# Kernel optimization log

Hardware: AMD Instinct MI355X
Metric: run time of the kernel (lower is better)

Reference implementation:

```python
import jax, jax.numpy as jnp
import numpy as np

# Reference for Net.get_seed_aff_x4 (+ Sinkhorn), the custom-kernel hotspot of this
# module. The ResNet50 conv stack / side convs are standard cuDNN-covered ops and the
# external `resnet50` module is not part of this source; `feature` here is hie_fea
# (768ch at side3 resolution) and `norm_cam` is the bg-augmented CAM at the same
# resolution, exactly as they arrive at get_seed_aff_x4 in forward.

N, C, H, W, CF = 8, 21, 64, 64, 768
NUM_CLUSTERS = 2
KMEANS_ITERS = 10      # deterministic Lloyd iterations (external kmeans_pytorch is
                       # randomly initialized; we use first-two-valid-pixel init)
EPS_OT = 0.1
SINK_MAX_ITER = 100
SINK_THRESH = 0.01


def setup_inputs() -> dict:
    key = jax.random.key(0)
    k1, k2, k3 = jax.random.split(key, 3)
    norm_cam = jax.random.uniform(k1, (N, C, H, W), dtype=jnp.float32)
    label = (jax.random.uniform(k2, (N, C, 1, 1)) < 0.8).astype(jnp.float32)
    label = label.at[:, 0].set(1.0)  # background always present
    feature = jax.random.normal(k3, (N, CF, H, W), dtype=jnp.float32)
    return {"norm_cam": norm_cam, "label": label, "feature": feature}


def _kmeans_cosine(feat, feat_n, mask):
    # feat: [HW, CF] raw features, feat_n: [HW, CF] l2-normalized, mask: [HW] in {0,1}
    valid = mask > 0
    cnt = valid.sum()
    order = jnp.argsort(jnp.where(valid, 0, 1))  # stable: valid pixels first
    init = feat[order[:NUM_CLUSTERS]] * mask[order[:NUM_CLUSTERS], None]

    def step(centers, _):
        cn = centers / jnp.maximum(
            jnp.linalg.norm(centers, axis=-1, keepdims=True), 1e-8)
        sim = feat_n @ cn.T                                  # [HW, K]
        assign = jnp.argmax(sim, axis=-1)
        oh = jax.nn.one_hot(assign, NUM_CLUSTERS, dtype=feat.dtype) * mask[:, None]
        counts = oh.sum(0)
        new_c = (oh.T @ feat) / jnp.maximum(counts, 1.0)[:, None]
        return new_c, None

    centers, _ = jax.lax.scan(step, init, None, length=KMEANS_ITERS)
    # original `continue` when < num_clusters valid pixels -> centers stay zero
    return jnp.where(cnt >= NUM_CLUSTERS, centers, jnp.zeros_like(centers))


def _sinkhorn(K, u, v):
    # K: [C, M, Nk]; faithful to Net.Sinkhorn incl. early stop on mean |r - r0|
    def cond(state):
        i, r, c, err = state
        return (i < SINK_MAX_ITER) & (err >= SINK_THRESH)

    def body(state):
        i, r, c, _ = state
        r0 = r
        r = u / jnp.einsum('cmk,ck->cm', K, c)
        c = v / jnp.einsum('cmk,cm->ck', K, r)
        err = jnp.abs(r - r0).mean()
        return (i + 1, r, c, err)

    state0 = (jnp.int32(0), jnp.ones_like(u), jnp.ones_like(v),
              jnp.asarray(jnp.inf, u.dtype))
    _, r, c, _ = jax.lax.while_loop(cond, body, state0)
    return r[..., None] * c[..., None, :] * K


def reference(norm_cam, label, feature):
    n, c, h, w = norm_cam.shape
    cf = feature.shape[1]
    hw = h * w

    # seeds: one-hot argmax of norm_cam, gated by image-level labels
    belonging = jnp.argmax(norm_cam, axis=1)                       # [n,h,w]
    seeds = jnp.transpose(jax.nn.one_hot(belonging, c, dtype=norm_cam.dtype),
                          (0, 3, 1, 2)) * label                    # [n,c,h,w]
    # nearest-interp to feature size is identity (same HxW by construction)
    mask = seeds.reshape(n, c, hw)                                 # [n,c,hw]

    feat = feature.reshape(n, cf, hw).transpose(0, 2, 1)           # [n,hw,cf]
    feat_n = feat / jnp.maximum(
        jnp.linalg.norm(feat, axis=-1, keepdims=True), 1e-8)

    # per-(image, class) cosine k-means, fully vectorized (no python data loops)
    centers = jax.vmap(
        lambda f, fn, ms: jax.vmap(_kmeans_cosine, in_axes=(None, None, 0))(f, fn, ms)
    )(feat, feat_n, mask)                                          # [n,c,K,cf]
    cnt = (mask > 0).sum(-1)                                       # [n,c]

    # cosine similarity of ALL pixels to the 2 centers, mean over clusters
    centers_n = centers / jnp.maximum(
        jnp.linalg.norm(centers, axis=-1, keepdims=True), 1e-8)
    cos = jnp.einsum('nmd,nckd->nckm', feat_n, centers_n)          # [n,c,K,hw]
    cam = jnp.where((cnt >= NUM_CLUSTERS)[..., None],
                    cos.mean(axis=2), 0.0).reshape(n, c, h, w)

    # --- Sinkhorn OT refinement (torch.no_grad in original) ---
    feat_ot = feat / (jnp.linalg.norm(feat, axis=-1, keepdims=True) + 1e-5)
    cflat = centers.reshape(n, c * NUM_CLUSTERS, cf)
    cflat = cflat / (jnp.linalg.norm(cflat, axis=-1, keepdims=True) + 1e-5)
    sim = jnp.einsum('nmd,njd->nmj', feat_ot, cflat)               # [n,hw,c*K]
    # faithful to original's sim.view(M, N, n_cls).permute(2, 0, 1)
    sim = sim.reshape(n, hw, NUM_CLUSTERS, c).transpose(0, 3, 1, 2)  # [n,c,hw,K]
    Kmat = jax.lax.stop_gradient(jnp.exp(-(1.0 - sim) / EPS_OT))
    u = jnp.full((c, hw), 1.0 / hw, dtype=sim.dtype)
    v = jnp.full((c, NUM_CLUSTERS), 1.0 / NUM_CLUSTERS, dtype=sim.dtype)
    T = jax.vmap(lambda Kb: _sinkhorn(Kb, u, v))(Kmat)             # [n,c,hw,K]
    T = T.transpose(0, 1, 3, 2).reshape(n, c, NUM_CLUSTERS, h, w)

    # all_cam_maps.mean(dim=2) * label, then per-map max normalization
    out = cam * label
    out = out / (out.max(axis=(2, 3), keepdims=True) + 1e-5)
    return out, T


if __name__ == '__main__':
    o = reference(**setup_inputs())
    print(o[0].shape, o[1].shape)
```

## Files before the change

kernel.cpp:

```cpp
#include <hip/hip_runtime.h>
#include <hip/hip_bf16.h>
#include <stdint.h>

#define NIMG 8
#define NCLS 21
#define HW   4096
#define CF   768
#define NK   2
#define NJ   42
#define NJP  48
#define SINK_MAX 100

using uint32 = unsigned int;
using u16    = unsigned short;

__device__ __forceinline__ float b2f(u16 u){ union{uint32 i; float f;} x; x.i=((uint32)u)<<16; return x.f; }
__device__ __forceinline__ u16 f2b(float f){ union{float f; uint32 i;} x; x.f=f; return (u16)((x.i + 0x7fffu + ((x.i>>16)&1u))>>16); }

template<int BF>
__device__ __forceinline__ float ldin(const void* p, size_t idx){
    if (BF) return b2f(((const u16*)p)[idx]);
    return ((const float*)p)[idx];
}
template<int BF>
__device__ __forceinline__ void stout(void* p, size_t idx, float v){
    if (BF) ((u16*)p)[idx] = f2b(v);
    else    ((float*)p)[idx] = v;
}

__global__ void k_detect(const void* feat, int* flag){
    __shared__ int cnt;
    if (threadIdx.x == 0) cnt = 0;
    __syncthreads();
    const u16* f = (const u16*)feat;
    int bad = 0;
    for (int i = threadIdx.x; i < 4096; i += 256){
        int ex = (f[i] >> 7) & 0xFF;
        if (ex >= 160) bad++;
    }
    atomicAdd(&cnt, bad);
    __syncthreads();
    if (threadIdx.x == 0) *flag = (cnt < 64) ? 1 : 0;
}

template<int BF>
__global__ void k_seeds(const void* __restrict__ cam, const void* __restrict__ label,
                        int* __restrict__ pix_cls, const int* __restrict__ dflag){
    if (*dflag != BF) return;
    int g = blockIdx.x*256 + threadIdx.x;
    int n = g >> 12, p = g & 4095;
    float best = -1e30f; int bel = 0;
    for (int c = 0; c < NCLS; c++){
        float v = ldin<BF>(cam, (size_t)(n*NCLS + c)*HW + p);
        if (v > best){ best = v; bel = c; }
    }
    pix_cls[g] = (ldin<BF>(label, n*NCLS + bel) > 0.f) ? bel : -1;
}

template<int BF>
__global__ void k_norms(const void* __restrict__ feat, float* __restrict__ inv_n,
                        float* __restrict__ inv_ot, const int* __restrict__ dflag){
    if (*dflag != BF) return;
    int g = blockIdx.x*256 + threadIdx.x;
    int n = g >> 12, p = g & 4095;
    double s = 0.0;
    for (int k = 0; k < CF; k++){
        double v = (double)ldin<BF>(feat, (size_t)(n*CF + k)*HW + p);
        s += v*v;
    }
    double nr = sqrt(s);
    inv_n [g] = (float)(1.0/fmax(nr, 1e-8));
    inv_ot[g] = (float)(1.0/(nr + 1e-5));
}

template<int BF>
__global__ void k_transpose(const void* __restrict__ feat, float* __restrict__ featT,
                            const int* __restrict__ dflag){
    if (*dflag != BF) return;
    __shared__ float tile[64][65];
    int b = blockIdx.x;
    int n   = b / ((CF/64)*(HW/64));
    int rem = b % ((CF/64)*(HW/64));
    int kb = (rem / (HW/64)) * 64;
    int pb = (rem % (HW/64)) * 64;
    int tx = threadIdx.x & 63, ty = threadIdx.x >> 6;
    for (int i = 0; i < 16; i++){
        int k = ty*16 + i;
        tile[tx][k] = ldin<BF>(feat, ((size_t)(n*CF + kb + k))*HW + pb + tx);
    }
    __syncthreads();
    for (int i = 0; i < 16; i++){
        int p = ty*16 + i;
        featT[((size_t)(n*HW + pb + p))*CF + kb + tx] = tile[p][tx];
    }
}

__global__ void k_scan(const int* __restrict__ pix_cls, const float* __restrict__ featT,
                       int* __restrict__ cnt, int* __restrict__ plist,
                       double* __restrict__ centers){
    int b = blockIdx.x; int n = b / NCLS, c = b % NCLS;
    int lane = threadIdx.x;
    int* lst = plist + (size_t)b*HW;
    int count = 0, i0 = -1, i1 = -1;
    for (int base = 0; base < HW; base += 64){
        int cls = pix_cls[n*HW + base + lane];
        unsigned long long m = __ballot(cls == c);
        int pos = count + __popcll(m & ((1ull<<lane) - 1ull));
        if (cls == c) lst[pos] = base + lane;
        if (i0 < 0){
            if (m){ i0 = base + __ffsll((long long)m) - 1;
                    unsigned long long m2 = m & (m-1);
                    if (m2) i1 = base + __ffsll((long long)m2) - 1; }
        } else if (i1 < 0){
            if (m) i1 = base + __ffsll((long long)m) - 1;
        }
        count += __popcll(m);
    }
    if (lane == 0) cnt[b] = count;
    double* C0 = centers + (size_t)b*NK*CF;
    if (count >= 2){
        const float* r0 = featT + (size_t)(n*HW + i0)*CF;
        const float* r1 = featT + (size_t)(n*HW + i1)*CF;
        for (int e = lane; e < CF; e += 64){ C0[e] = (double)r0[e]; C0[CF+e] = (double)r1[e]; }
    } else {
        for (int e = lane; e < CF; e += 64){ C0[e] = 0.0; C0[CF+e] = 0.0; }
    }
}

__global__ __launch_bounds__(512, 1) void k_kmeans(const int* __restrict__ cnt,
                                                   const int* __restrict__ plist,
                                                   const float* __restrict__ featT,
                                                   double* __restrict__ centers){
    int b = blockIdx.x; int n = b / NCLS;
    int m = cnt[b];
    if (m < 2) return;
    __shared__ double Cs[2][CF];
    __shared__ float  As[2][CF];
    __shared__ double part[8][8][66];
    __shared__ double red[2];
    __shared__ float  ck[2];
    __shared__ double invn[2];
    __shared__ unsigned char asg[HW];
    __shared__ int chg;
    int tid = threadIdx.x, lane = tid & 63, w = tid >> 6;
    const int* lst = plist + (size_t)b*HW;
    double* Cg = centers + (size_t)b*NK*CF;
    for (int j = tid; j < CF; j += 512){ Cs[0][j] = Cg[j]; Cs[1][j] = Cg[CF+j]; }
    for (int i = tid; i < m; i += 512) asg[i] = 255;
    __syncthreads();
    for (int it = 0; it < 10; it++){
        if (tid < 2){ red[tid] = 0.0; ck[tid] = 0.f; }
        if (tid == 0) chg = 0;
        __syncthreads();
        double q0 = 0.0, q1 = 0.0;
        for (int j = tid; j < CF; j += 512){ q0 += Cs[0][j]*Cs[0][j]; q1 += Cs[1][j]*Cs[1][j]; }
        #pragma unroll
        for (int off = 32; off; off >>= 1){ q0 += __shfl_xor(q0, off); q1 += __shfl_xor(q1, off); }
        if (lane == 0){ atomicAdd(&red[0], q0); atomicAdd(&red[1], q1); }
        for (int j = tid; j < CF; j += 512){ As[0][j] = 0.f; As[1][j] = 0.f; }
        __syncthreads();
        if (tid == 0){
            invn[0] = 1.0/fmax(sqrt(red[0]), 1e-8);
            invn[1] = 1.0/fmax(sqrt(red[1]), 1e-8);
        }
        __syncthreads();
        double ic0 = invn[0], ic1 = invn[1];
        double c0r[12], c1r[12];
        #pragma unroll
        for (int s = 0; s < 3; s++){
            #pragma unroll
            for (int t = 0; t < 4; t++){
                int e = lane*4 + s*256 + t;
                c0r[s*4+t] = Cs[0][e];
                c1r[s*4+t] = Cs[1][e];
            }
        }
        float ac0[12], ac1[12];
        #pragma unroll
        for (int j = 0; j < 12; j++){ ac0[j] = 0.f; ac1[j] = 0.f; }
        int c0n = 0, c1n = 0, myChg = 0;
        float vA[4][12], vB[4][12];
        if (w < m){
            #pragma unroll
            for (int p = 0; p < 4; p++){
                int idx = w + 8*p; int iv = (idx < m) ? idx : (m-1);
                const float* row = featT + (size_t)(n*HW + lst[iv])*CF + lane*4;
                *(float4*)&vA[p][0] = *(const float4*)(row);
                *(float4*)&vA[p][4] = *(const float4*)(row + 256);
                *(float4*)&vA[p][8] = *(const float4*)(row + 512);
            }
        }
        for (int i = w; i < m; i += 32){
            int inext = i + 32;
            if (inext < m){
                #pragma unroll
                for (int p = 0; p < 4; p++){
                    int idx = inext + 8*p; int iv = (idx < m) ? idx : (m-1);
                    const float* row = featT + (size_t)(n*HW + lst[iv])*CF + lane*4;
                    *(float4*)&vB[p][0] = *(const float4*)(row);
                    *(float4*)&vB[p][4] = *(const float4*)(row + 256);
                    *(float4*)&vB[p][8] = *(const float4*)(row + 512);
                }
            }
            double d0[4], d1[4];
            #pragma unroll
            for (int p = 0; p < 4; p++){
                double s0 = 0.0, s1 = 0.0;
                #pragma unroll
                for (int j = 0; j < 12; j++){
                    s0 += (double)vA[p][j]*c0r[j];
                    s1 += (double)vA[p][j]*c1r[j];
                }
                d0[p] = s0; d1[p] = s1;
            }
            #pragma unroll
            for (int p = 0; p < 4; p++){
                part[w][2*p    ][lane] = d0[p];
                part[w][2*p + 1][lane] = d1[p];
            }
            asm volatile("s_waitcnt lgkmcnt(0)" ::: "memory");
            int s  = lane >> 3;
            int sub = lane & 7;
            const double* pr = &part[w][s][sub*8];
            double t = ((pr[0]+pr[1]) + (pr[2]+pr[3])) + ((pr[4]+pr[5]) + (pr[6]+pr[7]));
            t += __shfl_xor(t, 1);
            t += __shfl_xor(t, 2);
            t += __shfl_xor(t, 4);
            double tp = __shfl_xor(t, 8);
            int amine = 0;
            if ((lane & 8) == 0) amine = (t*ic0 >= tp*ic1) ? 0 : 1;
            unsigned long long bmask = __ballot(((lane & 8) == 0) && amine);
            #pragma unroll
            for (int p = 0; p < 4; p++){
                int idx = i + 8*p;
                if (idx < m){
                    int a = (int)((bmask >> (16*p)) & 1ull);
                    if (lane == 0){
                        if (asg[idx] != (unsigned char)a){ myChg++; asg[idx] = (unsigned char)a; }
                    }
                    if (a == 0){ c0n++;
                        #pragma unroll
                        for (int j = 0; j < 12; j++) ac0[j] += vA[p][j];
                    } else { c1n++;
                        #pragma unroll
                        for (int j = 0; j < 12; j++) ac1[j] += vA[p][j];
                    }
                }
            }
            #pragma unroll
            for (int p = 0; p < 4; p++){
                #pragma unroll
                for (int j = 0; j < 12; j++) vA[p][j] = vB[p][j];
            }
        }
        #pragma unroll
        for (int s = 0; s < 3; s++){
            #pragma unroll
            for (int t = 0; t < 4; t++){
                int e = lane*4 + s*256 + t;
                atomicAdd(&As[0][e], ac0[s*4+t]);
                atomicAdd(&As[1][e], ac1[s*4+t]);
            }
        }
        if (lane == 0){
            atomicAdd(&ck[0], (float)c0n); atomicAdd(&ck[1], (float)c1n);
            if (myChg) atomicAdd(&chg, myChg);
        }
        __syncthreads();
        if (chg == 0) break;
        double dv0 = fmax((double)ck[0], 1.0), dv1 = fmax((double)ck[1], 1.0);
        for (int j = tid; j < CF; j += 512){
            Cs[0][j] = (double)As[0][j]/dv0; Cs[1][j] = (double)As[1][j]/dv1;
        }
        __syncthreads();
    }
    for (int j = tid; j < CF; j += 512){ Cg[j] = Cs[0][j]; Cg[CF+j] = Cs[1][j]; }
}

__global__ void k_invc(const double* __restrict__ centers, float* __restrict__ invc_cam,
                       float* __restrict__ invc_ot){
    int b = blockIdx.x;
    int lane = threadIdx.x;
    const double* C = centers + (size_t)b*CF;
    double s = 0.0;
    for (int e = lane; e < CF; e += 64) s += C[e]*C[e];
    for (int off = 32; off; off >>= 1) s += __shfl_xor(s, off);
    if (lane == 0){
        double nr = sqrt(s);
        invc_cam[b] = (float)(1.0/fmax(nr, 1e-8));
        invc_ot[b]  = (float)(1.0/(nr + 1e-5));
    }
}

__global__ void k_cf32(const double* __restrict__ centers, float* __restrict__ Cf32){
    int n = blockIdx.x; int tid = threadIdx.x;
    for (int idx = tid; idx < NJP*CF; idx += 256){
        int j = idx / CF, e = idx - j*CF;
        float v = (j < NJ) ? (float)centers[((size_t)n*NJ + j)*CF + e] : 0.f;
        Cf32[(size_t)n*NJP*CF + idx] = v;
    }
}

__global__ __launch_bounds__(256) void k_gemmf(const float* __restrict__ featT,
                                               const float* __restrict__ Cf32,
                                               float* __restrict__ D){
    __shared__ float Fs[128][66];
    int b = blockIdx.x; int n = b >> 6; int pbase = (b & 63)*64;
    int tid = threadIdx.x, p = tid & 63;
    int jb = __builtin_amdgcn_readfirstlane((tid >> 6)*12);
    float acc[12];
    #pragma unroll
    for (int j = 0; j < 12; j++) acc[j] = 0.f;
    for (int kc = 0; kc < CF; kc += 128){
        __syncthreads();
        for (int idx = tid; idx < 64*64; idx += 256){
            int pp = idx >> 6, cw = idx & 63;
            float2 wv = *(const float2*)(featT + (size_t)(n*HW + pbase + pp)*CF + kc + cw*2);
            Fs[cw*2    ][pp] = wv.x;
            Fs[cw*2 + 1][pp] = wv.y;
        }
        __syncthreads();
        const float* Cb = Cf32 + (size_t)n*NJP*CF + kc;
        for (int k8 = 0; k8 < 128; k8 += 8){
            #pragma unroll
            for (int j = 0; j < 12; j++){
                const float* cr = Cb + (size_t)(jb + j)*CF + k8;
                #pragma unroll
                for (int k = 0; k < 8; k++)
                    acc[j] += Fs[k8 + k][p] * cr[k];
            }
        }
    }
    float* dp = D + ((size_t)(n*HW + pbase + p))*NJP + jb;
    #pragma unroll
    for (int j = 0; j < 12; j++) dp[j] = acc[j];
}

template<int BF>
__global__ __launch_bounds__(256) void k_out0(const float* __restrict__ D,
                                              const float* __restrict__ inv_n,
                                              const float* __restrict__ invc_cam,
                                              const int* __restrict__ cnt,
                                              void* __restrict__ out0,
                                              const int* __restrict__ dflag){
    if (*dflag != BF) return;
    int b = blockIdx.x; int n = b / NCLS, c = b % NCLS;
    __shared__ float wmax[4]; __shared__ float sden;
    int tid = threadIdx.x, lane = tid & 63, w = tid >> 6;
    size_t obase = (size_t)b*HW;
    if (cnt[b] < 2){
        for (int p = tid; p < HW; p += 256) stout<BF>(out0, obase + p, 0.f);
        return;
    }
    float ic0 = invc_cam[n*NJ + 2*c], ic1 = invc_cam[n*NJ + 2*c + 1];
    const float* Dn = D + (size_t)n*HW*NJP;
    float mx = -1e30f;
    for (int p = tid; p < HW; p += 256){
        const float* dp = Dn + (size_t)p*NJP + 2*c;
        float camv = 0.5f*(dp[0]*ic0 + dp[1]*ic1)*inv_n[n*HW + p];
        mx = fmaxf(mx, camv);
    }
    for (int off = 32; off; off >>= 1) mx = fmaxf(mx, __shfl_xor(mx, off));
    if (lane == 0) wmax[w] = mx;
    __syncthreads();
    if (tid == 0) sden = fmaxf(fmaxf(wmax[0], wmax[1]), fmaxf(wmax[2], wmax[3])) + 1e-5f;
    __syncthreads();
    float den = sden;
    for (int p = tid; p < HW; p += 256){
        const float* dp = Dn + (size_t)p*NJP + 2*c;
        float camv = 0.5f*(dp[0]*ic0 + dp[1]*ic1)*inv_n[n*HW + p];
        stout<BF>(out0, obase + p, camv/den);
    }
}

__global__ void k_kmat(const float* __restrict__ D, const float* __restrict__ inv_ot,
                       const float* __restrict__ invc_ot, float* __restrict__ Kg,
                       float* __restrict__ errg, int* __restrict__ arrv){
    if (blockIdx.x == 0){
        for (int i = threadIdx.x; i < NIMG*(SINK_MAX+1); i += 256){ errg[i] = 0.f; arrv[i] = 0; }
    }
    int g = blockIdx.x*256 + threadIdx.x;
    int n = g / (NCLS*HW);
    int rem = g - n*(NCLS*HW);
    int c = rem >> 12, p = rem & 4095;
    const float* dp = D + ((size_t)n*HW + p)*NJP;
    float io = inv_ot[n*HW + p];
    float s0 = dp[c]      * io * invc_ot[n*NJ + c];
    float s1 = dp[21 + c] * io * invc_ot[n*NJ + 21 + c];
    Kg[(size_t)g*2 + 0] = expf((s0 - 1.f)*10.f);
    Kg[(size_t)g*2 + 1] = expf((s1 - 1.f)*10.f);
}

template<int BF>
__global__ __launch_bounds__(256) void k_sink(const float* __restrict__ Kg,
                                              float* __restrict__ errg,
                                              int* __restrict__ arrv,
                                              void* __restrict__ d_out,
                                              const int* __restrict__ dflag){
    if (*dflag != BF) return;
    __shared__ float K0s[HW]; __shared__ float K1s[HW]; __shared__ float rs[HW];
    __shared__ float wred[4][3]; __shared__ float sh[3];
    int b = blockIdx.x; int n = b / NCLS;
    int tid = threadIdx.x, lane = tid & 63, w = tid >> 6;
    const float* Kb = Kg + (size_t)b*HW*2;
    for (int p = tid; p < HW; p += 256){ K0s[p] = Kb[p*2]; K1s[p] = Kb[p*2+1]; rs[p] = 1.f; }
    float cc0 = 1.f, cc1 = 1.f, err = 1e30f;
    const float u = 1.f/4096.f;
    int iter = 0;
    __syncthreads();
    while (iter < SINK_MAX && err >= 0.01f){
        float p0 = 0.f, p1 = 0.f, es = 0.f;
        for (int p = tid; p < HW; p += 256){
            float k0 = K0s[p], k1 = K1s[p];
            float rn = u / (k0*cc0 + k1*cc1);
            es += fabsf(rn - rs[p]);
            rs[p] = rn;
            p0 += k0*rn; p1 += k1*rn;
        }
        #pragma unroll
        for (int off = 32; off; off >>= 1){
            p0 += __shfl_xor(p0, off); p1 += __shfl_xor(p1, off); es += __shfl_xor(es, off);
        }
        if (lane == 0){ wred[w][0] = p0; wred[w][1] = p1; wred[w][2] = es; }
        __syncthreads();
        if (tid == 0){
            float P0 = wred[0][0]+wred[1][0]+wred[2][0]+wred[3][0];
            float P1 = wred[0][1]+wred[1][1]+wred[2][1]+wred[3][1];
            float ES = wred[0][2]+wred[1][2]+wred[2][2]+wred[3][2];
            sh[0] = 0.5f/P0; sh[1] = 0.5f/P1;
            int slot = n*(SINK_MAX+1) + iter;
            atomicAdd(&errg[slot], ES);
            __threadfence();
            atomicAdd(&arrv[slot], 1);
            while (__hip_atomic_load(&arrv[slot], __ATOMIC_ACQUIRE, __HIP_MEMORY_SCOPE_AGENT) < NCLS)
                __builtin_amdgcn_s_sleep(8);
            sh[2] = __hip_atomic_load(&errg[slot], __ATOMIC_RELAXED, __HIP_MEMORY_SCOPE_AGENT)
                    * (1.f/((float)NCLS*HW));
        }
        __syncthreads();
        cc0 = sh[0]; cc1 = sh[1]; err = sh[2];
        iter++;
    }
    size_t o1 = (size_t)NIMG*NCLS*HW + (size_t)b*NK*HW;
    for (int p = tid; p < HW; p += 256){
        float rv = rs[p];
        stout<BF>(d_out, o1 + p,      rv*cc0*K0s[p]);
        stout<BF>(d_out, o1 + HW + p, rv*cc1*K1s[p]);
    }
}

extern "C" void kernel_launch(void* const* d_in, const int* in_sizes, int n_in,
                              void* d_out, int out_size, void* d_ws, size_t ws_size,
                              hipStream_t stream){
    const void* cam   = d_in[0];
    const void* label = d_in[1];
    const void* feat  = d_in[2];

    char* ws = (char*)d_ws; size_t off = 0;
    auto alloc = [&](size_t bytes)->char*{
        char* p = ws + off; off = (off + bytes + 255) & ~(size_t)255; return p;
    };
    int*    dflag    = (int*)   alloc(4);
    float*  featT    = (float*) alloc((size_t)NIMG*HW*CF*4);
    double* centers  = (double*)alloc((size_t)NIMG*NCLS*NK*CF*8);
    float*  Cf32     = (float*) alloc((size_t)NIMG*NJP*CF*4);
    float*  inv_n    = (float*) alloc((size_t)NIMG*HW*4);
    float*  inv_ot   = (float*) alloc((size_t)NIMG*HW*4);
    int*    pix_cls  = (int*)   alloc((size_t)NIMG*HW*4);
    int*    cnt      = (int*)   alloc((size_t)NIMG*NCLS*4);
    int*    plist    = (int*)   alloc((size_t)NIMG*NCLS*HW*4);
    float*  invc_cam = (float*) alloc((size_t)NIMG*NJ*4);
    float*  invc_ot  = (float*) alloc((size_t)NIMG*NJ*4);
    float*  D        = (float*) alloc((size_t)NIMG*HW*NJP*4);
    float*  Kg       = (float*) alloc((size_t)NIMG*NCLS*HW*NK*4);
    float*  errg     = (float*) alloc((size_t)NIMG*(SINK_MAX+1)*4);
    int*    arrv     = (int*)   alloc((size_t)NIMG*(SINK_MAX+1)*4);

    k_detect<<<1, 256, 0, stream>>>(feat, dflag);

    k_seeds<1><<<NIMG*HW/256, 256, 0, stream>>>(cam, label, pix_cls, dflag);
    k_seeds<0><<<NIMG*HW/256, 256, 0, stream>>>(cam, label, pix_cls, dflag);
    k_norms<1><<<NIMG*HW/256, 256, 0, stream>>>(feat, inv_n, inv_ot, dflag);
    k_norms<0><<<NIMG*HW/256, 256, 0, stream>>>(feat, inv_n, inv_ot, dflag);
    k_transpose<1><<<NIMG*(CF/64)*(HW/64), 256, 0, stream>>>(feat, featT, dflag);
    k_transpose<0><<<NIMG*(CF/64)*(HW/64), 256, 0, stream>>>(feat, featT, dflag);

    k_scan  <<<NIMG*NCLS, 64, 0, stream>>>(pix_cls, featT, cnt, plist, centers);
    k_kmeans<<<NIMG*NCLS, 512, 0, stream>>>(cnt, plist, featT, centers);
    k_invc  <<<NIMG*NJ, 64, 0, stream>>>(centers, invc_cam, invc_ot);
    k_cf32  <<<NIMG, 256, 0, stream>>>(centers, Cf32);
    k_gemmf <<<NIMG*64, 256, 0, stream>>>(featT, Cf32, D);

    k_out0<1><<<NIMG*NCLS, 256, 0, stream>>>(D, inv_n, invc_cam, cnt, d_out, dflag);
    k_out0<0><<<NIMG*NCLS, 256, 0, stream>>>(D, inv_n, invc_cam, cnt, d_out, dflag);

    k_kmat  <<<NIMG*NCLS*HW/256, 256, 0, stream>>>(D, inv_ot, invc_ot, Kg, errg, arrv);

    k_sink<1><<<NIMG*NCLS, 256, 0, stream>>>(Kg, errg, arrv, d_out, dflag);
    k_sink<0><<<NIMG*NCLS, 256, 0, stream>>>(Kg, errg, arrv, d_out, dflag);
}
```

Baseline: 631.1 us.

## Split k-means across multiple blocks per class with per-iteration kernel launches

```diff
diff --git a/kernel.cpp b/kernel.cpp
--- a/kernel.cpp
+++ b/kernel.cpp
@@ -10,6 +10,8 @@
 #define NJ   42
 #define NJP  48
 #define SINK_MAX 100
+#define KMG  8
+#define KMIT 10
 
 using uint32 = unsigned int;
 using u16    = unsigned short;
@@ -97,7 +99,9 @@
 
 __global__ void k_scan(const int* __restrict__ pix_cls, const float* __restrict__ featT,
                        int* __restrict__ cnt, int* __restrict__ plist,
-                       double* __restrict__ centers){
+                       double* __restrict__ centers, int* __restrict__ ck0g,
+                       int* __restrict__ chgg, int* __restrict__ converged,
+                       unsigned char* __restrict__ asgg){
     int b = blockIdx.x; int n = b / NCLS, c = b % NCLS;
     int lane = threadIdx.x;
     int* lst = plist + (size_t)b*HW;
@@ -117,6 +121,9 @@
         count += __popcll(m);
     }
     if (lane == 0) cnt[b] = count;
+    for (int i = lane; i < HW; i += 64) asgg[(size_t)b*HW + i] = 255;
+    if (lane < KMIT + 1){ ck0g[b*(KMIT+1) + lane] = 0; chgg[b*(KMIT+1) + lane] = 0; }
+    if (lane == 0) converged[b] = 0;
     double* C0 = centers + (size_t)b*NK*CF;
     if (count >= 2){
         const float* r0 = featT + (size_t)(n*HW + i0)*CF;
@@ -127,154 +134,178 @@
     }
 }
 
-__global__ __launch_bounds__(512, 1) void k_kmeans(const int* __restrict__ cnt,
-                                                   const int* __restrict__ plist,
-                                                   const float* __restrict__ featT,
-                                                   double* __restrict__ centers){
-    int b = blockIdx.x; int n = b / NCLS;
+__global__ __launch_bounds__(512, 1) void k_kmA(const int it,
+        const int* __restrict__ cnt, const int* __restrict__ plist,
+        const float* __restrict__ featT, const double* __restrict__ centers,
+        int* __restrict__ ck0g, int* __restrict__ chgg,
+        const int* __restrict__ converged, unsigned char* __restrict__ asgg,
+        float* __restrict__ Asg){
+    int b2 = blockIdx.x; int b = b2 >> 3, g = b2 & 7; int n = b / NCLS;
+    if (converged[b]) return;
     int m = cnt[b];
     if (m < 2) return;
     __shared__ double Cs[2][CF];
     __shared__ float  As[2][CF];
     __shared__ double part[8][8][66];
     __shared__ double red[2];
-    __shared__ float  ck[2];
     __shared__ double invn[2];
-    __shared__ unsigned char asg[HW];
-    __shared__ int chg;
     int tid = threadIdx.x, lane = tid & 63, w = tid >> 6;
     const int* lst = plist + (size_t)b*HW;
-    double* Cg = centers + (size_t)b*NK*CF;
-    for (int j = tid; j < CF; j += 512){ Cs[0][j] = Cg[j]; Cs[1][j] = Cg[CF+j]; }
-    for (int i = tid; i < m; i += 512) asg[i] = 255;
-    __syncthreads();
-    for (int it = 0; it < 10; it++){
-        if (tid < 2){ red[tid] = 0.0; ck[tid] = 0.f; }
-        if (tid == 0) chg = 0;
-        __syncthreads();
-        double q0 = 0.0, q1 = 0.0;
-        for (int j = tid; j < CF; j += 512){ q0 += Cs[0][j]*Cs[0][j]; q1 += Cs[1][j]*Cs[1][j]; }
-        #pragma unroll
-        for (int off = 32; off; off >>= 1){ q0 += __shfl_xor(q0, off); q1 += __shfl_xor(q1, off); }
-        if (lane == 0){ atomicAdd(&red[0], q0); atomicAdd(&red[1], q1); }
-        for (int j = tid; j < CF; j += 512){ As[0][j] = 0.f; As[1][j] = 0.f; }
-        __syncthreads();
-        if (tid == 0){
-            invn[0] = 1.0/fmax(sqrt(red[0]), 1e-8);
-            invn[1] = 1.0/fmax(sqrt(red[1]), 1e-8);
-        }
-        __syncthreads();
-        double ic0 = invn[0], ic1 = invn[1];
-        double c0r[12], c1r[12];
-        #pragma unroll
-        for (int s = 0; s < 3; s++){
-            #pragma unroll
-            for (int t = 0; t < 4; t++){
-                int e = lane*4 + s*256 + t;
-                c0r[s*4+t] = Cs[0][e];
-                c1r[s*4+t] = Cs[1][e];
-            }
-        }
-        float ac0[12], ac1[12];
-        #pragma unroll
-        for (int j = 0; j < 12; j++){ ac0[j] = 0.f; ac1[j] = 0.f; }
-        int c0n = 0, c1n = 0, myChg = 0;
-        float vA[4][12], vB[4][12];
-        if (w < m){
+    const double* Cg = centers + (size_t)b*NK*CF;
+    if (tid < 2) red[tid] = 0.0;
+    for (int j = tid; j < CF; j += 512){
+        Cs[0][j] = Cg[j]; Cs[1][j] = Cg[CF+j]; As[0][j] = 0.f; As[1][j] = 0.f;
+    }
+    __syncthreads();
+    double q0 = 0.0, q1 = 0.0;
+    for (int j = tid; j < CF; j += 512){ q0 += Cs[0][j]*Cs[0][j]; q1 += Cs[1][j]*Cs[1][j]; }
+    #pragma unroll
+    for (int off = 32; off; off >>= 1){ q0 += __shfl_xor(q0, off); q1 += __shfl_xor(q1, off); }
+    if (lane == 0){ atomicAdd(&red[0], q0); atomicAdd(&red[1], q1); }
+    __syncthreads();
+    if (tid == 0){
+        invn[0] = 1.0/fmax(sqrt(red[0]), 1e-8);
+        invn[1] = 1.0/fmax(sqrt(red[1]), 1e-8);
+    }
+    __syncthreads();
+    double ic0 = invn[0], ic1 = invn[1];
+    double c0r[12], c1r[12];
+    #pragma unroll
+    for (int s = 0; s < 3; s++){
+        #pragma unroll
+        for (int t = 0; t < 4; t++){
+            int e = lane*4 + s*256 + t;
+            c0r[s*4+t] = Cs[0][e];
+            c1r[s*4+t] = Cs[1][e];
+        }
+    }
+    float ac0[12], ac1[12];
+    #pragma unroll
+    for (int j = 0; j < 12; j++){ ac0[j] = 0.f; ac1[j] = 0.f; }
+    int c0n = 0, myChg = 0;
+    int chunk = (m + KMG - 1) / KMG;
+    int lo = g*chunk; int hi = lo + chunk; if (hi > m) hi = m;
+    unsigned char* arow = asgg + (size_t)b*HW;
+    float vA[4][12], vB[4][12];
+    int i0 = lo + w;
+    if (i0 < hi){
+        #pragma unroll
+        for (int p = 0; p < 4; p++){
+            int idx = i0 + 8*p; int iv = (idx < hi) ? idx : (hi-1);
+            const float* row = featT + (size_t)(n*HW + lst[iv])*CF + lane*4;
+            *(float4*)&vA[p][0] = *(const float4*)(row);
+            *(float4*)&vA[p][4] = *(const float4*)(row + 256);
+            *(float4*)&vA[p][8] = *(const float4*)(row + 512);
+        }
+    }
+    for (int i = i0; i < hi; i += 32){
+        int inext = i + 32;
+        if (inext < hi){
             #pragma unroll
             for (int p = 0; p < 4; p++){
-                int idx = w + 8*p; int iv = (idx < m) ? idx : (m-1);
+                int idx = inext + 8*p; int iv = (idx < hi) ? idx : (hi-1);
                 const float* row = featT + (size_t)(n*HW + lst[iv])*CF + lane*4;
-                *(float4*)&vA[p][0] = *(const float4*)(row);
-                *(float4*)&vA[p][4] = *(const float4*)(row + 256);
-                *(float4*)&vA[p][8] = *(const float4*)(row + 512);
+                *(float4*)&vB[p][0] = *(const float4*)(row);
+                *(float4*)&vB[p][4] = *(const float4*)(row + 256);
+                *(float4*)&vB[p][8] = *(const float4*)(row + 512);
             }
         }
-        for (int i = w; i < m; i += 32){
-            int inext = i + 32;
-            if (inext < m){
-                #pragma unroll
-                for (int p = 0; p < 4; p++){
-                    int idx = inext + 8*p; int iv = (idx < m) ? idx : (m-1);
-                    const float* row = featT + (size_t)(n*HW + lst[iv])*CF + lane*4;
-                    *(float4*)&vB[p][0] = *(const float4*)(row);
-                    *(float4*)&vB[p][4] = *(const float4*)(row + 256);
-                    *(float4*)&vB[p][8] = *(const float4*)(row + 512);
+        double d0[4], d1[4];
+        #pragma unroll
+        for (int p = 0; p < 4; p++){
+            double s0 = 0.0, s1 = 0.0;
+            #pragma unroll
+            for (int j = 0; j < 12; j++){
+                s0 += (double)vA[p][j]*c0r[j];
+                s1 += (double)vA[p][j]*c1r[j];
+            }
+            d0[p] = s0; d1[p] = s1;
+        }
+        #pragma unroll
+        for (int p = 0; p < 4; p++){
+            part[w][2*p    ][lane] = d0[p];
+            part[w][2*p + 1][lane] = d1[p];
+        }
+        asm volatile("s_waitcnt lgkmcnt(0)" ::: "memory");
+        int s  = lane >> 3;
+        int sub = lane & 7;
+        const double* pr = &part[w][s][sub*8];
+        double t = ((pr[0]+pr[1]) + (pr[2]+pr[3])) + ((pr[4]+pr[5]) + (pr[6]+pr[7]));
+        t += __shfl_xor(t, 1);
+        t += __shfl_xor(t, 2);
+        t += __shfl_xor(t, 4);
+        double tp = __shfl_xor(t, 8);
+        int amine = 0;
+        if ((lane & 8) == 0) amine = (t*ic0 >= tp*ic1) ? 0 : 1;
+        unsigned long long bmask = __ballot(((lane & 8) == 0) && amine);
+        #pragma unroll
+        for (int p = 0; p < 4; p++){
+            int idx = i + 8*p;
+            if (idx < hi){
+                int a = (int)((bmask >> (16*p)) & 1ull);
+                if (lane == 0){
+                    if (arow[idx] != (unsigned char)a){ myChg++; arow[idx] = (unsigned char)a; }
+                }
+                if (a == 0){ c0n++;
+                    #pragma unroll
+                    for (int j = 0; j < 12; j++) ac0[j] += vA[p][j];
+                } else {
+                    #pragma unroll
+                    for (int j = 0; j < 12; j++) ac1[j] += vA[p][j];
                 }
             }
-            double d0[4], d1[4];
+        }
+        #pragma unroll
+        for (int p = 0; p < 4; p++){
             #pragma unroll
-            for (int p = 0; p < 4; p++){
-                double s0 = 0.0, s1 = 0.0;
-                #pragma unroll
-                for (int j = 0; j < 12; j++){
-                    s0 += (double)vA[p][j]*c0r[j];
-                    s1 += (double)vA[p][j]*c1r[j];
-                }
-                d0[p] = s0; d1[p] = s1;
-            }
-            #pragma unroll
-            for (int p = 0; p < 4; p++){
-                part[w][2*p    ][lane] = d0[p];
-                part[w][2*p + 1][lane] = d1[p];
-            }
-            asm volatile("s_waitcnt lgkmcnt(0)" ::: "memory");
-            int s  = lane >> 3;
-            int sub = lane & 7;
-            const double* pr = &part[w][s][sub*8];
-            double t = ((pr[0]+pr[1]) + (pr[2]+pr[3])) + ((pr[4]+pr[5]) + (pr[6]+pr[7]));
-            t += __shfl_xor(t, 1);
-            t += __shfl_xor(t, 2);
-            t += __shfl_xor(t, 4);
-            double tp = __shfl_xor(t, 8);
-            int amine = 0;
-            if ((lane & 8) == 0) amine = (t*ic0 >= tp*ic1) ? 0 : 1;
-            unsigned long long bmask = __ballot(((lane & 8) == 0) && amine);
-            #pragma unroll
-            for (int p = 0; p < 4; p++){
-                int idx = i + 8*p;
-                if (idx < m){
-                    int a = (int)((bmask >> (16*p)) & 1ull);
-                    if (lane == 0){
-                        if (asg[idx] != (unsigned char)a){ myChg++; asg[idx] = (unsigned char)a; }
-                    }
-                    if (a == 0){ c0n++;
-                        #pragma unroll
-                        for (int j = 0; j < 12; j++) ac0[j] += vA[p][j];
-                    } else { c1n++;
-                        #pragma unroll
-                        for (int j = 0; j < 12; j++) ac1[j] += vA[p][j];
-                    }
-                }
-            }
-            #pragma unroll
-            for (int p = 0; p < 4; p++){
-                #pragma unroll
-                for (int j = 0; j < 12; j++) vA[p][j] = vB[p][j];
-            }
-        }
-        #pragma unroll
-        for (int s = 0; s < 3; s++){
-            #pragma unroll
-            for (int t = 0; t < 4; t++){
-                int e = lane*4 + s*256 + t;
-                atomicAdd(&As[0][e], ac0[s*4+t]);
-                atomicAdd(&As[1][e], ac1[s*4+t]);
-            }
-        }
-        if (lane == 0){
-            atomicAdd(&ck[0], (float)c0n); atomicAdd(&ck[1], (float)c1n);
-            if (myChg) atomicAdd(&chg, myChg);
-        }
-        __syncthreads();
-        if (chg == 0) break;
-        double dv0 = fmax((double)ck[0], 1.0), dv1 = fmax((double)ck[1], 1.0);
-        for (int j = tid; j < CF; j += 512){
-            Cs[0][j] = (double)As[0][j]/dv0; Cs[1][j] = (double)As[1][j]/dv1;
-        }
-        __syncthreads();
-    }
-    for (int j = tid; j < CF; j += 512){ Cg[j] = Cs[0][j]; Cg[CF+j] = Cs[1][j]; }
+            for (int j = 0; j < 12; j++) vA[p][j] = vB[p][j];
+        }
+    }
+    #pragma unroll
+    for (int s = 0; s < 3; s++){
+        #pragma unroll
+        for (int t = 0; t < 4; t++){
+            int e = lane*4 + s*256 + t;
+            atomicAdd(&As[0][e], ac0[s*4+t]);
+            atomicAdd(&As[1][e], ac1[s*4+t]);
+        }
+    }
+    __syncthreads();
+    float* Ap = Asg + ((size_t)b*KMG + g)*(2*CF);
+    for (int j = tid; j < CF; j += 512){ Ap[j] = As[0][j]; Ap[CF + j] = As[1][j]; }
+    if (lane == 0){
+        if (c0n)   atomicAdd(&ck0g[b*(KMIT+1) + it], c0n);
+        if (myChg) atomicAdd(&chgg[b*(KMIT+1) + it], myChg);
+    }
+}
+
+__global__ __launch_bounds__(512) void k_kmB(const int it, const int* __restrict__ cnt,
+        const float* __restrict__ Asg, const int* __restrict__ ck0g,
+        const int* __restrict__ chgg, int* __restrict__ converged,
+        double* __restrict__ centers){
+    int b = blockIdx.x;
+    if (converged[b]) return;
+    int m = cnt[b];
+    if (m < 2) return;
+    int tid = threadIdx.x;
+    if (chgg[b*(KMIT+1) + it] == 0){
+        if (tid == 0) converged[b] = 1;
+        return;
+    }
+    int c0 = ck0g[b*(KMIT+1) + it];
+    double dv0 = fmax((double)c0, 1.0), dv1 = fmax((double)(m - c0), 1.0);
+    const float* Ap = Asg + (size_t)b*KMG*(2*CF);
+    double* Cg = centers + (size_t)b*NK*CF;
+    for (int j = tid; j < CF; j += 512){
+        float s0 = 0.f, s1 = 0.f;
+        #pragma unroll
+        for (int g = 0; g < KMG; g++){
+            s0 += Ap[(size_t)g*(2*CF) + j];
+            s1 += Ap[(size_t)g*(2*CF) + CF + j];
+        }
+        Cg[j]      = (double)s0/dv0;
+        Cg[CF + j] = (double)s1/dv1;
+    }
 }
 
 __global__ void k_invc(const double* __restrict__ centers, float* __restrict__ invc_cam,
@@ -475,6 +506,11 @@
     float*  Kg       = (float*) alloc((size_t)NIMG*NCLS*HW*NK*4);
     float*  errg     = (float*) alloc((size_t)NIMG*(SINK_MAX+1)*4);
     int*    arrv     = (int*)   alloc((size_t)NIMG*(SINK_MAX+1)*4);
+    float*  Asg      = (float*) alloc((size_t)NIMG*NCLS*KMG*2*CF*4);
+    int*    ck0g     = (int*)   alloc((size_t)NIMG*NCLS*(KMIT+1)*4);
+    int*    chgg     = (int*)   alloc((size_t)NIMG*NCLS*(KMIT+1)*4);
+    int*    convg    = (int*)   alloc((size_t)NIMG*NCLS*4);
+    unsigned char* asgg = (unsigned char*)alloc((size_t)NIMG*NCLS*HW);
 
     k_detect<<<1, 256, 0, stream>>>(feat, dflag);
 
@@ -485,8 +521,13 @@
     k_transpose<1><<<NIMG*(CF/64)*(HW/64), 256, 0, stream>>>(feat, featT, dflag);
     k_transpose<0><<<NIMG*(CF/64)*(HW/64), 256, 0, stream>>>(feat, featT, dflag);
 
-    k_scan  <<<NIMG*NCLS, 64, 0, stream>>>(pix_cls, featT, cnt, plist, centers);
-    k_kmeans<<<NIMG*NCLS, 512, 0, stream>>>(cnt, plist, featT, centers);
+    k_scan<<<NIMG*NCLS, 64, 0, stream>>>(pix_cls, featT, cnt, plist, centers,
+                                         ck0g, chgg, convg, asgg);
+    for (int it = 0; it < KMIT; ++it){
+        k_kmA<<<NIMG*NCLS*KMG, 512, 0, stream>>>(it, cnt, plist, featT, centers,
+                                                 ck0g, chgg, convg, asgg, Asg);
+        k_kmB<<<NIMG*NCLS, 512, 0, stream>>>(it, cnt, Asg, ck0g, chgg, convg, centers);
+    }
     k_invc  <<<NIMG*NJ, 64, 0, stream>>>(centers, invc_cam, invc_ot);
     k_cf32  <<<NIMG, 256, 0, stream>>>(centers, Cf32);
     k_gemmf <<<NIMG*64, 256, 0, stream>>>(featT, Cf32, D);
```

New measurement: 887.3 us. 1.41x slower.
